# Kernel tuning notes

Hardware: AMD Instinct MI355X
Metric: run time of the kernel (lower is better)

The kernel has to match this reference:

```python
import jax, jax.numpy as jnp
import numpy as np

NUM_HEADS = 10
LN_EPS = 1e-5


def setup_inputs() -> dict:
    key = jax.random.key(0)
    ks = jax.random.split(key, 6)
    N, D = 4096, 640  # in_dim == out_dim required by residual add
    x = jax.random.normal(ks[0], (N, D), dtype=jnp.float32)
    s = 1.0 / np.sqrt(D)
    Wq = jax.random.normal(ks[1], (D, D), dtype=jnp.float32) * s  # torch Linear weight [out,in]
    Wk = jax.random.normal(ks[2], (D, D), dtype=jnp.float32) * s
    Wv = jax.random.normal(ks[3], (D, D), dtype=jnp.float32) * s
    gamma = jnp.ones((D,), dtype=jnp.float32)
    beta = jnp.zeros((D,), dtype=jnp.float32)
    return {"x": x, "Wq": Wq, "Wk": Wk, "Wv": Wv, "gamma": gamma, "beta": beta}


def reference(x, Wq, Wk, Wv, gamma, beta):
    N, D = x.shape
    dk = D // NUM_HEADS
    Q = x @ Wq.T  # [N, D]
    K = x @ Wk.T
    V = x @ Wv.T
    # Faithful to source: raw reshapes (NOT transposes)
    Qh = Q.reshape(NUM_HEADS, N, dk)
    Kh = K.reshape(NUM_HEADS, N, dk).reshape(NUM_HEADS, dk, N)  # torch.reshape, not .mT
    Vh = V.reshape(NUM_HEADS, N, dk)
    # Faithful quirk: scale by sqrt(K.shape[2]) == sqrt(N)
    scale = np.float32(np.sqrt(N))
    wghts = jax.nn.softmax((Qh @ Kh) / scale, axis=-1)  # [H, N, N]
    values = wghts @ Vh  # [H, N, dk]
    values = values.reshape(N, NUM_HEADS * dk)  # raw reshape merge
    values = values + x  # residual
    # LayerNorm(out_dim), biased variance, eps=1e-5
    mean = jnp.mean(values, axis=-1, keepdims=True)
    var = jnp.mean(jnp.square(values - mean), axis=-1, keepdims=True)
    out = (values - mean) * jax.lax.rsqrt(var + LN_EPS) * gamma + beta
    return out
```

## Files before the change

### kernel.cpp

```cpp
#include <hip/hip_runtime.h>
#if __has_include(<hip/hip_fp8.h>)
#include <hip/hip_fp8.h>
#endif


typedef __bf16 bf16x8 __attribute__((ext_vector_type(8)));
typedef __bf16 bf16x4 __attribute__((ext_vector_type(4)));
typedef float  f32x4  __attribute__((ext_vector_type(4)));
typedef unsigned short u16x4 __attribute__((ext_vector_type(4)));
typedef unsigned int   u32x4 __attribute__((ext_vector_type(4)));
typedef long           la64  __attribute__((may_alias));
typedef unsigned int   ua32  __attribute__((may_alias));

#define N_TOK   4096
#define D_MODEL 640
#define DK      64
#define HSLAB   (N_TOK * DK)
#define SQS 0.15014030f

#if __has_builtin(__builtin_amdgcn_exp2f)
#define EXP2(x) __builtin_amdgcn_exp2f(x)
#else
#define EXP2(x) exp2f(x)
#endif

__device__ __forceinline__ void stage16(const void* g, void* lds_uniform) {
    __builtin_amdgcn_global_load_lds(
        (const __attribute__((address_space(1))) unsigned int*)g,
        (__attribute__((address_space(3))) unsigned int*)lds_uniform, 16, 0, 0);
}

__device__ __forceinline__ u16x4 cvt4(f32x4 v) {
    return __builtin_bit_cast(u16x4, __builtin_convertvector(v, bf16x4));
}

__device__ __forceinline__ unsigned int pk_fp8(f32x4 v) {
#if __has_builtin(__builtin_amdgcn_cvt_pk_fp8_f32)
    int r = 0;
    r = __builtin_amdgcn_cvt_pk_fp8_f32(v[0], v[1], r, false);
    r = __builtin_amdgcn_cvt_pk_fp8_f32(v[2], v[3], r, true);
    return (unsigned int)r;
#else
    union { unsigned char b[4]; unsigned int u; } x;
    x.b[0] = __hip_fp8_e4m3(v[0]).__x;
    x.b[1] = __hip_fp8_e4m3(v[1]).__x;
    x.b[2] = __hip_fp8_e4m3(v[2]).__x;
    x.b[3] = __hip_fp8_e4m3(v[3]).__x;
    return x.u;
#endif
}

__global__ __launch_bounds__(256) void cvt_all(const float* __restrict__ x,
                                               const float* __restrict__ w0,
                                               const float* __restrict__ w1,
                                               const float* __restrict__ w2,
                                               unsigned short* __restrict__ xb,
                                               unsigned short* __restrict__ d0,
                                               unsigned short* __restrict__ d1,
                                               unsigned short* __restrict__ d2,
                                               f32x4* __restrict__ ltot4) {
    int i = blockIdx.x * 256 + threadIdx.x;
    if (i >= 962560) { ltot4[i - 962560] = (f32x4){0.f, 0.f, 0.f, 0.f}; return; }
    const float* s; unsigned short* d; int off; float scl = 1.0f;
    if (i < 655360) { s = x; d = xb; off = i; }
    else {
        int j = i - 655360;
        int w = j / 102400; off = j - w * 102400;
        s = (w == 0) ? w0 : (w == 1) ? w1 : w2;
        d = (w == 0) ? d0 : (w == 1) ? d1 : d2;
        if (w < 2) scl = SQS;
    }
    f32x4 v = ((const f32x4*)s)[off];
    v[0] *= scl; v[1] *= scl; v[2] *= scl; v[3] *= scl;
    ((u16x4*)d)[off] = cvt4(v);
}

__global__ __launch_bounds__(256, 2) void gemm_qkv(
    const unsigned short* __restrict__ xb,
    const unsigned short* __restrict__ wq,
    const unsigned short* __restrict__ wk,
    const unsigned short* __restrict__ wv,
    unsigned char*  __restrict__ Qf8o,
    unsigned short* __restrict__ Ko,
    unsigned short* __restrict__ Vo) {
    const int b = blockIdx.x;
    const int g = b & 31;
    const int r = b >> 5;
    const int mode = r / 5;
    const int m0 = g * 128;
    const int n0 = (r % 5) * 128;
    const unsigned short* W = (mode == 0) ? wq : (mode == 1) ? wk : wv;
    unsigned short*       C = (mode == 1) ? Ko : Vo;

    __shared__ unsigned short As[8192];
    __shared__ unsigned short Bs[8192];

    const int tid  = threadIdx.x;
    const int lane = tid & 63;
    const int wave = tid >> 6;
    const int quad = lane >> 4, l16 = lane & 15;
    const int wm = (wave >> 1) * 64, wn = (wave & 1) * 64;
    const int swz = l16 & 7;

    f32x4 acc[4][4] = {};

    int prow[4], pcol[4], lbase[4];
    for (int j = 0; j < 4; j++) {
        int p = j * 256 + tid;
        prow[j] = p >> 3;
        pcol[j] = ((p & 7) ^ (prow[j] & 7)) * 8;
        lbase[j] = (j * 256 + wave * 64) * 8;
    }

    for (int kt = 0; kt < D_MODEL; kt += 64) {
        __syncthreads();
        for (int j = 0; j < 4; j++) {
            stage16(&xb[(size_t)(m0 + prow[j]) * D_MODEL + kt + pcol[j]], As + lbase[j]);
            stage16(&W [(size_t)(n0 + prow[j]) * D_MODEL + kt + pcol[j]], Bs + lbase[j]);
        }
        __syncthreads();

        for (int s = 0; s < 2; s++) {
            bf16x8 af[4], bfr[4];
            for (int mi = 0; mi < 4; mi++) {
                int row = wm + mi * 16 + l16;
                af[mi] = *(const bf16x8*)&As[row * 64 + (((s << 2) + quad) ^ swz) * 8];
            }
            for (int ni = 0; ni < 4; ni++) {
                int row = wn + ni * 16 + l16;
                bfr[ni] = *(const bf16x8*)&Bs[row * 64 + (((s << 2) + quad) ^ swz) * 8];
            }
            for (int mi = 0; mi < 4; mi++)
                for (int ni = 0; ni < 4; ni++)
                    acc[mi][ni] = __builtin_amdgcn_mfma_f32_16x16x32_bf16(af[mi], bfr[ni], acc[mi][ni], 0, 0, 0);
        }
    }

    if (mode == 0) {
        for (int mi = 0; mi < 4; mi++)
            for (int ni = 0; ni < 4; ni++) {
                unsigned int p = pk_fp8(acc[mi][ni]);
                for (int r2 = 0; r2 < 4; r2++) {
                    int row = m0 + wm + mi * 16 + quad * 4 + r2;
                    int col = n0 + wn + ni * 16 + l16;
                    Qf8o[(size_t)row * D_MODEL + col] = (unsigned char)(p >> (r2 * 8));
                }
            }
    } else {
        for (int mi = 0; mi < 4; mi++)
            for (int ni = 0; ni < 4; ni++) {
                u16x4 cv = cvt4(acc[mi][ni]);
                for (int r2 = 0; r2 < 4; r2++) {
                    int row = m0 + wm + mi * 16 + quad * 4 + r2;
                    int col = n0 + wn + ni * 16 + l16;
                    C[(size_t)row * D_MODEL + col] = cv[r2];
                }
            }
    }
}

__global__ __launch_bounds__(256) void transpose_kv(
    const unsigned short* __restrict__ Kn, unsigned char* __restrict__ Kp8,
    const unsigned short* __restrict__ Vn, unsigned char* __restrict__ Vp8) {
    const int z = blockIdx.z;
    const int t = threadIdx.x;

    __shared__ unsigned short T[64][66];
    const unsigned short* src; unsigned char* dst;
    int R, Cc, r0, c0;
    if (z < 10) { src = Kn; dst = Kp8; R = 64;   Cc = 4096; r0 = 0; c0 = blockIdx.x * 64; }
    else        { src = Vn; dst = Vp8; R = 4096; Cc = 64;   r0 = blockIdx.x * 64; c0 = 0; }
    const size_t hb = (size_t)(z % 10) * HSLAB;
    const int rr = t >> 3, c8 = (t & 7) * 8;

    for (int hf = 0; hf < 2; hf++) {
        int r = rr + hf * 32;
        bf16x8 v = *(const bf16x8*)&src[hb + (size_t)(r0 + r) * Cc + c0 + c8];
        for (int j = 0; j < 8; j++) T[r][c8 + j] = ((unsigned short*)&v)[j];
    }
    __syncthreads();
    const bf16x8 zz = {};
    for (int hf = 0; hf < 2; hf++) {
        int r = rr + hf * 32;
        *(bf16x8*)&((unsigned short*)src)[hb + (size_t)(r0 + r) * Cc + c0 + c8] = zz;
    }
    for (int hf = 0; hf < 2; hf++) {
        int oc = rr + hf * 32;
        f32x4 lo, hi;
        for (int j = 0; j < 4; j++) {
            lo[j] = __builtin_bit_cast(float, (unsigned int)T[c8 + j][oc] << 16);
            hi[j] = __builtin_bit_cast(float, (unsigned int)T[c8 + 4 + j][oc] << 16);
        }
        uint2 ov; ov.x = pk_fp8(lo); ov.y = pk_fp8(hi);
        size_t dcol = (z < 10) ? ((size_t)(c0 + oc) * 64 + r0 + c8)
                               : ((size_t)oc * 4096 + r0 + c8);
        *(uint2*)&dst[hb + dcol] = ov;
    }
}

__global__ __launch_bounds__(256, 4) void attn(
    const unsigned char* __restrict__ Qf8,
    const unsigned char* __restrict__ Kp8,
    const unsigned char* __restrict__ Vp8,
    float* __restrict__ vals,
    float* __restrict__ l_tot) {
    const int h  = blockIdx.x >> 5;
    const int qt = blockIdx.x & 31;
    const int tile0 = blockIdx.y * 16;
    const int lane = threadIdx.x & 63;
    const int wave = threadIdx.x >> 6;
    const int quad = lane >> 4, l16 = lane & 15;
    const size_t hoff = (size_t)h * HSLAB;

    __shared__ unsigned char sm[20480];
    unsigned char* const Kb0 = sm;
    unsigned char* const Kb1 = sm + 4096;
    unsigned char* const Vt  = sm + 8192;
    unsigned char* const Pw  = sm + 12288 + wave * 2048;

    const int qbase = qt * 128 + wave * 32;
    long qd[2][2];
    for (int g = 0; g < 2; g++) {
        const unsigned char* qp = Qf8 + hoff + (size_t)(qbase + g * 16 + l16) * 64 + quad * 8;
        qd[g][0] = *(const la64*)(qp);
        qd[g][1] = *(const la64*)(qp + 32);
    }

    f32x4 o[2][4] = {};
    f32x4 ol[2] = {};
    const long ONES8 = 0x3838383838383838L;

    const int c = wave * 64 + lane;
    const int kKey = ((c >> 5) << 3) + (c & 7), kCi = (c >> 3) & 3;

    const int fb = (l16 >> 3) * 512 + (quad >> 1) * 128 + (l16 & 7) * 16 + (quad & 1) * 8;

    {
        const int keyb = tile0 << 6;
        stage16(Kp8 + hoff + (size_t)(keyb + kKey) * 64 + kCi * 16, Kb0 + wave * 1024);
    }

    for (int t = 0; t < 16; t++) {
        const int keyb = (tile0 + t) << 6;
        unsigned char* const Kcur = (t & 1) ? Kb1 : Kb0;

        __syncthreads();

        if (t + 1 < 16) {
            const int keyn = (tile0 + t + 1) << 6;
            unsigned char* const Knext = (t & 1) ? Kb0 : Kb1;
            stage16(Kp8 + hoff + (size_t)(keyn + kKey) * 64 + kCi * 16, Knext + wave * 1024);
        }
        stage16(Vp8 + hoff + (size_t)kKey * N_TOK + keyb + kCi * 16, Vt + wave * 1024);

        for (int ni = 0; ni < 4; ni++) {
            const unsigned char* kp = Kcur + ni * 1024 + fb;
            long a0 = *(const la64*)(kp);
            long a1 = *(const la64*)(kp + 256);
            for (int g = 0; g < 2; g++) {
                f32x4 s = {};
                __builtin_amdgcn_s_setprio(1);
                s = __builtin_amdgcn_mfma_f32_16x16x32_fp8_fp8(a0, qd[g][0], s, 0, 0, 0);
                s = __builtin_amdgcn_mfma_f32_16x16x32_fp8_fp8(a1, qd[g][1], s, 0, 0, 0);
                __builtin_amdgcn_s_setprio(0);
                f32x4 pv;
                for (int r = 0; r < 4; r++) pv[r] = EXP2(s[r]);
                const int pu = ni * 2 + (quad >> 1);
                *(ua32*)(Pw + pu * 256 +
                         (((g * 16 + l16) + ((pu & 3) << 3)) & 31) * 8 +
                         (quad & 1) * 4) = pk_fp8(pv);
            }
        }

        __syncthreads();

        for (int ks = 0; ks < 2; ks++) {
            long vf[4];
            for (int nd = 0; nd < 4; nd++)
                vf[nd] = *(const la64*)(Vt + nd * 1024 + ks * 256 + fb);
            for (int g = 0; g < 2; g++) {
                long pf = *(const la64*)(Pw + (ks * 4 + quad) * 256 +
                                         (((g * 16 + l16) + (quad << 3)) & 31) * 8);
                __builtin_amdgcn_s_setprio(1);
                ol[g] = __builtin_amdgcn_mfma_f32_16x16x32_fp8_fp8(pf, ONES8, ol[g], 0, 0, 0);
                for (int nd = 0; nd < 4; nd++)
                    o[g][nd] = __builtin_amdgcn_mfma_f32_16x16x32_fp8_fp8(pf, vf[nd], o[g][nd], 0, 0, 0);
                __builtin_amdgcn_s_setprio(0);
            }
        }
    }

    if (l16 == 0)
        for (int g = 0; g < 2; g++)
            for (int r = 0; r < 4; r++)
                atomicAdd(&l_tot[(h << 12) + qbase + g * 16 + quad * 4 + r], ol[g][r]);

    for (int g = 0; g < 2; g++)
        for (int nd = 0; nd < 4; nd++)
            for (int r = 0; r < 4; r++) {
                int q = qbase + g * 16 + quad * 4 + r;
                atomicAdd(&vals[hoff + (size_t)q * DK + nd * 16 + l16], o[g][nd][r]);
            }
}

__global__ __launch_bounds__(256) void ln_kernel(
    const float* __restrict__ vals, const float* __restrict__ l_tot,
    const float* __restrict__ x,
    const float* __restrict__ gamma, const float* __restrict__ beta,
    float* __restrict__ out) {
    const int wave = threadIdx.x >> 6, lane = threadIdx.x & 63;
    const int row  = blockIdx.x * 4 + wave;
    const float* v  = vals + (size_t)row * D_MODEL;
    const float* xr = x    + (size_t)row * D_MODEL;

    float t[10];
    float s = 0.f;
    for (int i = 0; i < 10; i++) {
        float linv = 1.0f / l_tot[row * 10 + i];
        t[i] = v[lane + i * 64] * linv + xr[lane + i * 64];
        s += t[i];
    }
    for (int off = 32; off; off >>= 1) s += __shfl_xor(s, off, 64);
    float mean = s * (1.0f / 640.0f);
    float s2 = 0.f;
    for (int i = 0; i < 10; i++) { float d = t[i] - mean; s2 += d * d; }
    for (int off = 32; off; off >>= 1) s2 += __shfl_xor(s2, off, 64);
    float inv = rsqrtf(s2 * (1.0f / 640.0f) + 1e-5f);

    float* orow = out + (size_t)row * D_MODEL;
    for (int i = 0; i < 10; i++) {
        int c = lane + i * 64;
        orow[c] = (t[i] - mean) * inv * gamma[c] + beta[c];
    }
}

extern "C" void kernel_launch(void* const* d_in, const int* in_sizes, int n_in,
                              void* d_out, int out_size, void* d_ws, size_t ws_size,
                              hipStream_t stream) {
    const float* x     = (const float*)d_in[0];
    const float* Wq    = (const float*)d_in[1];
    const float* Wk    = (const float*)d_in[2];
    const float* Wv    = (const float*)d_in[3];
    const float* gamma = (const float*)d_in[4];
    const float* beta  = (const float*)d_in[5];
    float* out = (float*)d_out;

    char* ws = (char*)d_ws;
    unsigned short* xb  = (unsigned short*)(ws);
    unsigned short* wqb = (unsigned short*)(ws + 5242880);
    unsigned short* wkb = (unsigned short*)(ws + 6062080);
    unsigned short* wvb = (unsigned short*)(ws + 6881280);
    unsigned char*  Qf8 = (unsigned char*)(ws + 7700480);
    unsigned char*  Kp8 = (unsigned char*)(ws + 12943360);
    unsigned char*  Vp8 = (unsigned char*)(ws + 18186240);
    unsigned short* Kn  = (unsigned short*)(ws + 23429120);
    unsigned short* Vn  = (unsigned short*)(ws + 28672000);
    float*          vals  = (float*)(ws + 23429120);
    float*          l_tot = (float*)(ws + 33914880);

    cvt_all<<<3800, 256, 0, stream>>>(x, Wq, Wk, Wv, xb, wqb, wkb, wvb,
                                      (f32x4*)l_tot);

    gemm_qkv<<<480, 256, 0, stream>>>(xb, wqb, wkb, wvb, Qf8, Kn, Vn);

    transpose_kv<<<dim3(64, 1, 20), 256, 0, stream>>>(Kn, Kp8, Vn, Vp8);

    attn<<<dim3(320, 4), 256, 0, stream>>>(Qf8, Kp8, Vp8, vals, l_tot);
    ln_kernel<<<1024, 256, 0, stream>>>(vals, l_tot, x, gamma, beta, out);
}
```

Before: 157.6 us.

## Widen attention key tile to 128 and split keys three ways

The attention kernel now processes 128 keys per iteration instead of 64 and splits the key range into 3 chunks (11/11/10 tiles) rather than 4, so the grid shrinks from 320x4 to 320x3 blocks. K prefetch switches from double-buffered LDS async loads to register loads that are written into a single LDS buffer after the second barrier. LDS grows to 32KB per block. This halves the number of barriers per key and cuts per-block overhead and atomics, at the cost of more LDS and registers, which may lower occupancy. The grid also becomes less even across CUs.

```diff
diff --git a/kernel.cpp b/kernel.cpp
--- a/kernel.cpp
+++ b/kernel.cpp
@@ -9,6 +9,7 @@
 typedef float  f32x4  __attribute__((ext_vector_type(4)));
 typedef unsigned short u16x4 __attribute__((ext_vector_type(4)));
 typedef unsigned int   u32x4 __attribute__((ext_vector_type(4)));
+typedef u32x4          u32x4a __attribute__((may_alias));
 typedef long           la64  __attribute__((may_alias));
 typedef unsigned int   ua32  __attribute__((may_alias));
 
@@ -206,17 +207,17 @@
     float* __restrict__ l_tot) {
     const int h  = blockIdx.x >> 5;
     const int qt = blockIdx.x & 31;
-    const int tile0 = blockIdx.y * 16;
+    const int ntile = (blockIdx.y == 2) ? 10 : 11;
+    const int tile0 = blockIdx.y * 11;
     const int lane = threadIdx.x & 63;
     const int wave = threadIdx.x >> 6;
     const int quad = lane >> 4, l16 = lane & 15;
     const size_t hoff = (size_t)h * HSLAB;
 
-    __shared__ unsigned char sm[20480];
-    unsigned char* const Kb0 = sm;
-    unsigned char* const Kb1 = sm + 4096;
-    unsigned char* const Vt  = sm + 8192;
-    unsigned char* const Pw  = sm + 12288 + wave * 2048;
+    __shared__ unsigned char sm[32768];
+    unsigned char* const Kb = sm;
+    unsigned char* const Vt = sm + 8192;
+    unsigned char* const Pw = sm + 16384 + wave * 4096;
 
     const int qbase = qt * 128 + wave * 32;
     long qd[2][2];
@@ -230,31 +231,38 @@
     f32x4 ol[2] = {};
     const long ONES8 = 0x3838383838383838L;
 
-    const int c = wave * 64 + lane;
-    const int kKey = ((c >> 5) << 3) + (c & 7), kCi = (c >> 3) & 3;
-
-    const int fb = (l16 >> 3) * 512 + (quad >> 1) * 128 + (l16 & 7) * 16 + (quad & 1) * 8;
+    const int cA = wave * 64 + lane, cB = cA + 256;
+    const int kKeyA = ((cA >> 5) << 3) + (cA & 7), kCiA = (cA >> 3) & 3;
+    const int kKeyB = ((cB >> 5) << 3) + (cB & 7), kCiB = (cB >> 3) & 3;
+    const int vDkA  = ((cA >> 6) << 3) + (cA & 7), vCvA = (cA >> 3) & 7;
+    const int vDkB  = ((cB >> 6) << 3) + (cB & 7), vCvB = (cB >> 3) & 7;
+
+    const int kfb = (l16 >> 3) * 512 + (quad >> 1) * 128 + (l16 & 7) * 16 + (quad & 1) * 8;
+    const int vfb = (l16 >> 3) * 1024 + (quad >> 1) * 128 + (l16 & 7) * 16 + (quad & 1) * 8;
 
     {
-        const int keyb = tile0 << 6;
-        stage16(Kp8 + hoff + (size_t)(keyb + kKey) * 64 + kCi * 16, Kb0 + wave * 1024);
-    }
-
-    for (int t = 0; t < 16; t++) {
-        const int keyb = (tile0 + t) << 6;
-        unsigned char* const Kcur = (t & 1) ? Kb1 : Kb0;
+        const int keyb = tile0 << 7;
+        stage16(Kp8 + hoff + (size_t)(keyb + kKeyA) * 64 + kCiA * 16, Kb + wave * 1024);
+        stage16(Kp8 + hoff + (size_t)(keyb + kKeyB) * 64 + kCiB * 16, Kb + 4096 + wave * 1024);
+    }
+
+    for (int t = 0; t < ntile; t++) {
+        const int keyb = (tile0 + t) << 7;
 
         __syncthreads();
 
-        if (t + 1 < 16) {
-            const int keyn = (tile0 + t + 1) << 6;
-            unsigned char* const Knext = (t & 1) ? Kb0 : Kb1;
-            stage16(Kp8 + hoff + (size_t)(keyn + kKey) * 64 + kCi * 16, Knext + wave * 1024);
-        }
-        stage16(Vp8 + hoff + (size_t)kKey * N_TOK + keyb + kCi * 16, Vt + wave * 1024);
-
-        for (int ni = 0; ni < 4; ni++) {
-            const unsigned char* kp = Kcur + ni * 1024 + fb;
+        u32x4 kr0, kr1;
+        const bool pf_k = (t + 1 < ntile);
+        if (pf_k) {
+            const int keyn = (tile0 + t + 1) << 7;
+            kr0 = *(const u32x4a*)(Kp8 + hoff + (size_t)(keyn + kKeyA) * 64 + kCiA * 16);
+            kr1 = *(const u32x4a*)(Kp8 + hoff + (size_t)(keyn + kKeyB) * 64 + kCiB * 16);
+        }
+        stage16(Vp8 + hoff + (size_t)vDkA * N_TOK + keyb + vCvA * 16, Vt + wave * 1024);
+        stage16(Vp8 + hoff + (size_t)vDkB * N_TOK + keyb + vCvB * 16, Vt + 4096 + wave * 1024);
+
+        for (int ni = 0; ni < 8; ni++) {
+            const unsigned char* kp = Kb + ni * 1024 + kfb;
             long a0 = *(const la64*)(kp);
             long a1 = *(const la64*)(kp + 256);
             for (int g = 0; g < 2; g++) {
@@ -274,10 +282,15 @@
 
         __syncthreads();
 
-        for (int ks = 0; ks < 2; ks++) {
+        if (pf_k) {
+            *(u32x4a*)(Kb + (size_t)cA * 16) = kr0;
+            *(u32x4a*)(Kb + (size_t)cB * 16) = kr1;
+        }
+
+        for (int ks = 0; ks < 4; ks++) {
             long vf[4];
             for (int nd = 0; nd < 4; nd++)
-                vf[nd] = *(const la64*)(Vt + nd * 1024 + ks * 256 + fb);
+                vf[nd] = *(const la64*)(Vt + nd * 2048 + ks * 256 + vfb);
             for (int g = 0; g < 2; g++) {
                 long pf = *(const la64*)(Pw + (ks * 4 + quad) * 256 +
                                          (((g * 16 + l16) + (quad << 3)) & 31) * 8);
@@ -365,6 +378,6 @@
 
     transpose_kv<<<dim3(64, 1, 20), 256, 0, stream>>>(Kn, Kp8, Vn, Vp8);
 
-    attn<<<dim3(320, 4), 256, 0, stream>>>(Qf8, Kp8, Vp8, vals, l_tot);
+    attn<<<dim3(320, 3), 256, 0, stream>>>(Qf8, Kp8, Vp8, vals, l_tot);
     ln_kernel<<<1024, 256, 0, stream>>>(vals, l_tot, x, gamma, beta, out);
 }
```

Result: faster. 151.9 us (-3.6%).
